# Performance work log

Hardware: AMD Instinct MI355X
Metric: run time of the kernel (lower is better)

## Reference

```python
import jax, jax.numpy as jnp
import numpy as np

B, T, D, P, ALPHA, PR = 4, 4096, 1024, 512, 4, 64


def setup_inputs() -> dict:
    key = jax.random.key(0)
    ks = jax.random.split(key, 9)
    g = lambda k, shape, scale: jax.random.normal(k, shape, jnp.float32) * scale
    return {
        "x": jax.random.normal(ks[0], (B, T, D), jnp.float32),
        "W_toP": g(ks[1], (D, P), D ** -0.5),
        "W_U": g(ks[2], (D, P, ALPHA), D ** -0.5),
        "W_F": g(ks[3], (D, P), D ** -0.5),
        "W_V": g(ks[4], (P, ALPHA), 1.0),
        "W_lam": g(ks[5], (P, PR), P ** -0.5),
        "B_mat": g(ks[6], (P, PR), P ** -0.5),
        "C_mat": g(ks[7], (PR, P), PR ** -0.5),
        "W_fromP": g(ks[8], (P, D), P ** -0.5),
    }


def reference(x, W_toP, W_U, W_F, W_V, W_lam, B_mat, C_mat, W_fromP):
    # dense pre-path: (B,T,D)->(B,T,P)
    pre = jnp.einsum('btd,dp->btp', x, W_toP)
    # CeptaEmbedding dense pathway: multi-factor projection U, gates F, weighted Y
    U = jnp.einsum('btd,dpa->btpa', x, W_U)            # (B,T,P,alpha)
    Fg = jax.nn.sigmoid(jnp.einsum('btd,dp->btp', x, W_F))  # (B,T,P) in (0,1)
    Y = U * W_V                                        # (B,T,P,alpha)
    # CeptaRouting(reduce='sum'): sum over alpha factors, plus residual pre-path
    t = Y.sum(-1) + pre                                # (B,T,P)
    # CeptaSSMLowRank: input-dependent diagonal decay in rank-PR state space
    lam = jax.nn.sigmoid(jnp.einsum('btp,pr->btr', Fg, W_lam))  # (B,T,PR)
    u_in = jnp.einsum('btp,pr->btr', t, B_mat)                  # (B,T,PR)

    def step(s, inp):
        l, u = inp
        s = l * s + u
        return s, s

    s0 = jnp.zeros((x.shape[0], PR), x.dtype)
    _, s_seq = jax.lax.scan(step, s0, (lam.transpose(1, 0, 2), u_in.transpose(1, 0, 2)))
    s_seq = s_seq.transpose(1, 0, 2)                   # (B,T,PR)
    t_tilde = t + jnp.einsum('btr,rp->btp', s_seq, C_mat)
    h = jnp.einsum('btp,pd->btd', t_tilde, W_fromP)    # dropout p=0 -> identity
    return h
```

## Files before the change

kernel.cpp:

```cpp
#include <hip/hip_runtime.h>
#include <hip/hip_bf16.h>

#define Bb 4
#define Tt 4096
#define Dd 1024
#define Pp 512
#define PRr 64
#define Mm (Bb*Tt)
#define NCH 256
#define CL  16

typedef __bf16 bf16;
typedef __bf16 bf16x8 __attribute__((ext_vector_type(8)));
typedef __bf16 bf16x4 __attribute__((ext_vector_type(4)));
typedef float f32x4 __attribute__((ext_vector_type(4)));

#define GPTR(p) (const __attribute__((address_space(1))) void*)(p)
#define LPTR(p) (__attribute__((address_space(3))) void*)(p)

__device__ __forceinline__ float sigmoidf_(float x) {
    return 1.0f / (1.0f + __expf(-x));
}


__global__ void prep_w1(const float* __restrict__ W_toP, const float* __restrict__ W_U,
                        const float* __restrict__ W_V, const float* __restrict__ W_F,
                        bf16* __restrict__ W1t) {
    int idx = blockIdx.x * 256 + threadIdx.x;
    int n = idx >> 10, k = idx & 1023;
    float v;
    if (n < Pp) {
        int p = n;
        float4 u  = *(const float4*)(W_U + ((size_t)k * Pp + p) * 4);
        float4 wv = *(const float4*)(W_V + (size_t)p * 4);
        v = W_toP[(size_t)k * Pp + p] + u.x * wv.x + u.y * wv.y + u.z * wv.z + u.w * wv.w;
    } else {
        v = W_F[(size_t)k * Pp + (n - Pp)];
    }
    W1t[idx] = (bf16)v;
}

__global__ void prep_w3(const float* __restrict__ B_mat, const float* __restrict__ W_lam,
                        bf16* __restrict__ W3t) {
    int idx = blockIdx.x * 256 + threadIdx.x;
    int n = idx >> 10, k = idx & 1023;
    float v = 0.0f;
    if (n < PRr) { if (k < Pp) v = B_mat[(size_t)k * PRr + n]; }
    else         { if (k >= Pp) v = W_lam[(size_t)(k - Pp) * PRr + (n - PRr)]; }
    W3t[idx] = (bf16)v;
}

__global__ void zero_cw(float* __restrict__ CW) {
    int i = blockIdx.x * 256 + threadIdx.x;
    ((f32x4*)CW)[i] = (f32x4){};
}

__global__ void prep_cw(const float* __restrict__ C_mat, const float* __restrict__ W_fromP,
                        float* __restrict__ CW) {
    __shared__ float crow[64];
    int nc = blockIdx.x;
    int r  = blockIdx.y;
    int pc = blockIdx.z;
    int tid = threadIdx.x;
    if (tid < 64) crow[tid] = C_mat[(size_t)r * Pp + pc * 64 + tid];
    __syncthreads();
    int n = nc * 256 + tid;
    float acc = 0.0f;
    #pragma unroll 8
    for (int i = 0; i < 64; ++i)
        acc = fmaf(crow[i], W_fromP[(size_t)(pc * 64 + i) * Dd + n], acc);
    atomicAdd(&CW[(size_t)r * Dd + n], acc);
}

__global__ void prep_w2(const float* __restrict__ W_fromP, const float* __restrict__ CW,
                        bf16* __restrict__ W2t) {
    int n = blockIdx.x;
    int k = threadIdx.x;
    float v = (k < Pp) ? W_fromP[(size_t)k * Dd + n]
                       : CW[(size_t)(k - Pp) * Dd + n];
    W2t[(size_t)n * 576 + k] = (bf16)v;
}

__global__ void cast_x(const float* __restrict__ x, bf16* __restrict__ xb) {
    int i = blockIdx.x * 256 + threadIdx.x;
    float4 v = ((const float4*)x)[i];
    bf16x4 o;
    o[0] = (bf16)v.x; o[1] = (bf16)v.y; o[2] = (bf16)v.z; o[3] = (bf16)v.w;
    ((bf16x4*)xb)[i] = o;
}

__global__ void scan_phase1(const float* __restrict__ UL,
                            float* __restrict__ slocal, float* __restrict__ pprod,
                            float* __restrict__ carryS, float* __restrict__ carryP) {
    int b = blockIdx.y;
    int c = blockIdx.x * 4 + (threadIdx.x >> 6);
    int r = threadIdx.x & 63;
    const float* ulb = UL + ((size_t)b * Tt + (size_t)c * CL) * 128;
    float* sl = slocal + ((size_t)b * Tt + (size_t)c * CL) * PRr;
    float* pp = pprod  + ((size_t)b * Tt + (size_t)c * CL) * PRr;
    float uv[CL], lv[CL];
    #pragma unroll
    for (int i = 0; i < CL; i++) {
        uv[i] = ulb[(size_t)i * 128 + r];
        lv[i] = ulb[(size_t)i * 128 + 64 + r];
    }
    float s = 0.0f, p = 1.0f;
    #pragma unroll
    for (int i = 0; i < CL; i++) {
        s = fmaf(lv[i], s, uv[i]);
        p *= lv[i];
        sl[(size_t)i * PRr + r] = s;
        pp[(size_t)i * PRr + r] = p;
    }
    int ci = b * NCH + c;
    carryS[(size_t)ci * PRr + r] = s;
    carryP[(size_t)ci * PRr + r] = p;
}

__global__ void scan_phase2(const float* __restrict__ carryS, const float* __restrict__ carryP,
                            float* __restrict__ carryIn) {
    int b = blockIdx.x, r = threadIdx.x;
    float carry = 0.0f;
    for (int c0 = 0; c0 < NCH; c0 += 16) {
        float cs[16], cp[16];
        #pragma unroll
        for (int i = 0; i < 16; i++) {
            size_t idx = ((size_t)b * NCH + c0 + i) * PRr + r;
            cs[i] = carryS[idx];
            cp[i] = carryP[idx];
        }
        #pragma unroll
        for (int i = 0; i < 16; i++) {
            carryIn[((size_t)b * NCH + c0 + i) * PRr + r] = carry;
            carry = fmaf(cp[i], carry, cs[i]);
        }
    }
}

__global__ void scan_phase3(const float* __restrict__ slocal, const float* __restrict__ pprod,
                            const float* __restrict__ carryIn, bf16* __restrict__ sb) {
    int i = blockIdx.x * 256 + threadIdx.x;
    int r = i & (PRr - 1);
    int row = i >> 6;
    int b = row >> 12;
    int t = row & (Tt - 1);
    int c = t / CL;
    float carry = carryIn[((size_t)b * NCH + c) * PRr + r];
    sb[i] = (bf16)fmaf(pprod[i], carry, slocal[i]);
}

template <int EPI>
__global__ __launch_bounds__(512, 2) void gemm256(
    const bf16* __restrict__ A0, int lda0,
    const bf16* __restrict__ A1, int lda1, int ksplit,
    const bf16* __restrict__ Bt, int ldb, int K,
    void* __restrict__ Cout, int ldc, int sigcol) {

    __shared__ bf16 As[2][256 * 64];
    __shared__ bf16 Bs[2][256 * 64];

    const int tid  = threadIdx.x;
    const int lane = tid & 63;
    const int wid  = tid >> 6;
    const int wm   = wid >> 2;
    const int wn   = wid & 3;

    const int cpx = gridDim.x >> 3;
    const int bid = blockIdx.x;
    const int swz = (bid & 7) * cpx + (bid >> 3);
    const int mBase = (swz >> 2) * 256;
    const int nBase = (swz & 3) * 256;

    const int lr  = lane & 15;
    const int q16 = (lane >> 4) * 16;

    auto srcA = [&](int kt, const bf16*& src, int& lda, int& kc) {
        if (kt < ksplit) { src = A0; lda = lda0; kc = kt; }
        else             { src = A1; lda = lda1; kc = kt - ksplit; }
    };

    auto stage = [&](const bf16* src, int lda, int kc, int rowBase, bf16* lbuf, int rd) {
        int d = rd * 8192 + tid * 16;
        int L = d ^ (((d >> 7) & 7) << 4);
        int r = L >> 7;
        int c = (L & 127) >> 1;
        const bf16* g = src + (size_t)(rowBase + r) * lda + (kc + c);
        __builtin_amdgcn_global_load_lds(GPTR(g), LPTR((char*)lbuf + d), 16, 0, 0);
    };

    auto frag = [&](const bf16* lbuf, int r, int cb) -> bf16x8 {
        int flat = r * 128 + cb;
        int phys = flat ^ (((flat >> 7) & 7) << 4);
        return *(const bf16x8*)((const char*)lbuf + phys);
    };

    const int NT = K / 64;

    {
        const bf16* sa; int la, kc; srcA(0, sa, la, kc);
        stage(sa, la, kc, mBase, As[0], 0); stage(sa, la, kc, mBase, As[0], 2);
        stage(Bt, ldb, 0, nBase, Bs[0], 0); stage(Bt, ldb, 0, nBase, Bs[0], 1);
        stage(Bt, ldb, 0, nBase, Bs[0], 2); stage(Bt, ldb, 0, nBase, Bs[0], 3);
        stage(sa, la, kc, mBase, As[0], 1); stage(sa, la, kc, mBase, As[0], 3);
    }
    asm volatile("s_waitcnt vmcnt(2)" ::: "memory");
    __builtin_amdgcn_s_barrier();

    f32x4 acc[8][4] = {};
    bf16x8 a[4], b0[4], b1[4];

    for (int t = 0; t < NT; ++t) {
        bf16* Ac = As[t & 1];       bf16* Bc = Bs[t & 1];
        bf16* An = As[(t + 1) & 1]; bf16* Bn = Bs[(t + 1) & 1];
        const bool hn = (t + 1 < NT);
        const bf16* sa = A0; int la = lda0, kc = 0;
        if (hn) srcA((t + 1) * 64, sa, la, kc);
        const int ktn = (t + 1) * 64;

        #pragma unroll
        for (int i = 0; i < 4; ++i) a[i]  = frag(Ac, wm * 128 + i * 16 + lr, q16);
        #pragma unroll
        for (int i = 0; i < 4; ++i) b0[i] = frag(Bc, wn * 64 + i * 16 + lr, q16);
        if (hn) {
            stage(sa, la, kc, mBase, An, 0); stage(sa, la, kc, mBase, An, 2);
            asm volatile("s_waitcnt vmcnt(2)" ::: "memory");
        } else {
            asm volatile("s_waitcnt vmcnt(0)" ::: "memory");
        }
        __builtin_amdgcn_s_barrier();
        __builtin_amdgcn_s_setprio(1);
        #pragma unroll
        for (int m = 0; m < 4; ++m)
            #pragma unroll
            for (int n = 0; n < 4; ++n)
                acc[m][n] = __builtin_amdgcn_mfma_f32_16x16x32_bf16(a[m], b0[n], acc[m][n], 0, 0, 0);
        __builtin_amdgcn_s_setprio(0);
        __builtin_amdgcn_s_barrier();

        #pragma unroll
        for (int i = 0; i < 4; ++i) a[i] = frag(Ac, wm * 128 + (i + 4) * 16 + lr, q16);
        if (hn) { stage(Bt, ldb, ktn, nBase, Bn, 0); stage(Bt, ldb, ktn, nBase, Bn, 1); }
        __builtin_amdgcn_s_barrier();
        __builtin_amdgcn_s_setprio(1);
        #pragma unroll
        for (int m = 0; m < 4; ++m)
            #pragma unroll
            for (int n = 0; n < 4; ++n)
                acc[m + 4][n] = __builtin_amdgcn_mfma_f32_16x16x32_bf16(a[m], b0[n], acc[m + 4][n], 0, 0, 0);
        __builtin_amdgcn_s_setprio(0);
        __builtin_amdgcn_s_barrier();

        #pragma unroll
        for (int i = 0; i < 4; ++i) a[i]  = frag(Ac, wm * 128 + i * 16 + lr, 64 + q16);
        #pragma unroll
        for (int i = 0; i < 4; ++i) b1[i] = frag(Bc, wn * 64 + i * 16 + lr, 64 + q16);
        if (hn) { stage(Bt, ldb, ktn, nBase, Bn, 2); stage(Bt, ldb, ktn, nBase, Bn, 3); }
        __builtin_amdgcn_s_barrier();
        __builtin_amdgcn_s_setprio(1);
        #pragma unroll
        for (int m = 0; m < 4; ++m)
            #pragma unroll
            for (int n = 0; n < 4; ++n)
                acc[m][n] = __builtin_amdgcn_mfma_f32_16x16x32_bf16(a[m], b1[n], acc[m][n], 0, 0, 0);
        __builtin_amdgcn_s_setprio(0);
        __builtin_amdgcn_s_barrier();

        #pragma unroll
        for (int i = 0; i < 4; ++i) a[i] = frag(Ac, wm * 128 + (i + 4) * 16 + lr, 64 + q16);
        if (hn) {
            stage(sa, la, kc, mBase, An, 1); stage(sa, la, kc, mBase, An, 3);
            asm volatile("s_waitcnt vmcnt(2)" ::: "memory");
        }
        __builtin_amdgcn_s_barrier();
        __builtin_amdgcn_s_setprio(1);
        #pragma unroll
        for (int m = 0; m < 4; ++m)
            #pragma unroll
            for (int n = 0; n < 4; ++n)
                acc[m + 4][n] = __builtin_amdgcn_mfma_f32_16x16x32_bf16(a[m], b1[n], acc[m + 4][n], 0, 0, 0);
        __builtin_amdgcn_s_setprio(0);
        __builtin_amdgcn_s_barrier();
    }

    const int lr4 = (lane >> 4) * 4;
    #pragma unroll
    for (int m = 0; m < 8; ++m) {
        #pragma unroll
        for (int n = 0; n < 4; ++n) {
            #pragma unroll
            for (int j = 0; j < 4; ++j) {
                int row = mBase + wm * 128 + m * 16 + lr4 + j;
                int col = nBase + wn * 64 + n * 16 + lr;
                float v = acc[m][n][j];
                if (EPI == 0) {
                    if (col >= sigcol) v = sigmoidf_(v);
                    ((bf16*)Cout)[(size_t)row * ldc + col] = (bf16)v;
                } else {
                    ((float*)Cout)[(size_t)row * ldc + col] = v;
                }
            }
        }
    }
}

template <int EPI>
__global__ __launch_bounds__(256) void gemm_bt(
    const bf16* __restrict__ A0, int lda0,
    const bf16* __restrict__ A1, int lda1, int ksplit,
    const bf16* __restrict__ Bt, int K,
    void* __restrict__ Cout, int ldc, int sigcol) {

    __shared__ bf16 As[128][32];
    __shared__ bf16 Bs[128][32];

    const int tid  = threadIdx.x;
    const int lane = tid & 63;
    const int wid  = tid >> 6;
    const int wr   = (wid >> 1) * 64;
    const int wc   = (wid & 1) * 64;
    const int mBase = blockIdx.x * 128;
    const int nBase = blockIdx.y * 128;

    f32x4 acc[4][4] = {};

    const int lr = lane & 15;
    const int lk = (lane >> 4) * 8;

    for (int kt = 0; kt < K; kt += 32) {
        const bf16* Asrc; int lda_; int kcol;
        if (kt < ksplit) { Asrc = A0; lda_ = lda0; kcol = kt; }
        else             { Asrc = A1; lda_ = lda1; kcol = kt - ksplit; }

        __syncthreads();
        #pragma unroll
        for (int i = 0; i < 2; i++) {
            int c = tid + i * 256;
            int row = c >> 2, k8 = (c & 3) * 8;
            const bf16* g = Asrc + (size_t)(mBase + row) * lda_ + (kcol + k8);
            __builtin_amdgcn_global_load_lds(GPTR(g), LPTR(&As[0][0] + c * 8), 16, 0, 0);
        }
        #pragma unroll
        for (int i = 0; i < 2; i++) {
            int c = tid + i * 256;
            int row = c >> 2, k8 = (c & 3) * 8;
            const bf16* g = Bt + (size_t)(nBase + row) * K + (kt + k8);
            __builtin_amdgcn_global_load_lds(GPTR(g), LPTR(&Bs[0][0] + c * 8), 16, 0, 0);
        }
        __syncthreads();

        bf16x8 af[4], bfr[4];
        #pragma unroll
        for (int m = 0; m < 4; m++) af[m]  = *(const bf16x8*)(&As[wr + m * 16 + lr][lk]);
        #pragma unroll
        for (int n = 0; n < 4; n++) bfr[n] = *(const bf16x8*)(&Bs[wc + n * 16 + lr][lk]);
        #pragma unroll
        for (int m = 0; m < 4; m++)
            #pragma unroll
            for (int n = 0; n < 4; n++)
                acc[m][n] = __builtin_amdgcn_mfma_f32_16x16x32_bf16(af[m], bfr[n], acc[m][n], 0, 0, 0);
    }

    const int lr4 = (lane >> 4) * 4;
    const int lc  = lane & 15;
    #pragma unroll
    for (int m = 0; m < 4; m++) {
        #pragma unroll
        for (int n = 0; n < 4; n++) {
            #pragma unroll
            for (int j = 0; j < 4; j++) {
                int row = mBase + wr + m * 16 + lr4 + j;
                int col = nBase + wc + n * 16 + lc;
                float v = acc[m][n][j];
                if (EPI == 1) {
                    if (col >= sigcol) v = sigmoidf_(v);
                    ((float*)Cout)[(size_t)row * ldc + col] = v;
                } else {
                    ((float*)Cout)[(size_t)row * ldc + col] = v;
                }
            }
        }
    }
}

extern "C" void kernel_launch(void* const* d_in, const int* in_sizes, int n_in,
                              void* d_out, int out_size, void* d_ws, size_t ws_size,
                              hipStream_t stream) {
    const float* x       = (const float*)d_in[0];
    const float* W_toP   = (const float*)d_in[1];
    const float* W_U     = (const float*)d_in[2];
    const float* W_F     = (const float*)d_in[3];
    const float* W_V     = (const float*)d_in[4];
    const float* W_lam   = (const float*)d_in[5];
    const float* B_mat   = (const float*)d_in[6];
    const float* C_mat   = (const float*)d_in[7];
    const float* W_fromP = (const float*)d_in[8];
    float* out = (float*)d_out;

    char* ws = (char*)d_ws;
    size_t off = 0;
    auto alloc = [&](size_t bytes) { void* p = ws + off; off = (off + bytes + 255) & ~255ULL; return p; };
    bf16*  xb  = (bf16*)alloc((size_t)Mm * Dd * 2);
    bf16*  TF  = (bf16*)alloc((size_t)Mm * 1024 * 2);
    float* UL  = (float*)alloc((size_t)Mm * 128 * 4);
    bf16*  sb  = (bf16*)alloc((size_t)Mm * PRr * 2);
    bf16*  W1t = (bf16*)alloc((size_t)1024 * 1024 * 2);
    bf16*  W3t = (bf16*)alloc((size_t)128 * 1024 * 2);
    bf16*  W2t = (bf16*)alloc((size_t)1024 * 576 * 2);
    float* CW  = (float*)alloc((size_t)PRr * Dd * 4);
    float* slocal = (float*)alloc((size_t)Mm * PRr * 4);
    float* pprod  = (float*)alloc((size_t)Mm * PRr * 4);
    float* carryS = (float*)alloc((size_t)Bb * NCH * PRr * 4);
    float* carryP = (float*)alloc((size_t)Bb * NCH * PRr * 4);
    float* carryI = (float*)alloc((size_t)Bb * NCH * PRr * 4);

    prep_w1<<<dim3(4096), dim3(256), 0, stream>>>(W_toP, W_U, W_V, W_F, W1t);
    prep_w3<<<dim3(512),  dim3(256), 0, stream>>>(B_mat, W_lam, W3t);
    zero_cw<<<dim3(64),   dim3(256), 0, stream>>>(CW);
    prep_cw<<<dim3(4, 64, 8), dim3(256), 0, stream>>>(C_mat, W_fromP, CW);
    prep_w2<<<dim3(1024), dim3(576), 0, stream>>>(W_fromP, CW, W2t);
    cast_x <<<dim3(Mm * Dd / 4 / 256), dim3(256), 0, stream>>>(x, xb);

    gemm256<0><<<dim3((Mm / 256) * (1024 / 256)), 512, 0, stream>>>(
        xb, Dd, xb, Dd, 1 << 30, W1t, Dd, Dd, TF, 1024, Pp);

    gemm_bt<1><<<dim3(Mm / 128, 1), 256, 0, stream>>>(
        TF, 1024, TF, 1024, 1 << 30, W3t, 1024, UL, 128, PRr);

    scan_phase1<<<dim3(NCH / 4, Bb), dim3(256), 0, stream>>>(UL, slocal, pprod, carryS, carryP);
    scan_phase2<<<dim3(Bb), dim3(PRr), 0, stream>>>(carryS, carryP, carryI);
    scan_phase3<<<dim3(Mm * PRr / 256), dim3(256), 0, stream>>>(slocal, pprod, carryI, sb);

    gemm256<2><<<dim3((Mm / 256) * (1024 / 256)), 512, 0, stream>>>(
        TF, 1024, sb, PRr, Pp, W2t, 576, 576, out, Dd, 1 << 30);
}
```

Before: 159.1 us.

## Replace 256x256 pipelined GEMM with simpler 128x128 gemm_bt kernel for both big GEMMs

Removes the hand-pipelined 256x256-tile gemm256 kernel and runs the two large GEMMs through the existing 128x128-tile gemm_bt kernel, adding a bf16 sigmoid epilogue variant to it. It also folds the CW zeroing kernel into prep_w3 as extra blocks, saving one launch. The smaller tiles and missing software pipelining likely lower MFMA efficiency and data reuse, in exchange for more blocks and simpler code.

```diff
diff --git a/kernel.cpp b/kernel.cpp
--- a/kernel.cpp
+++ b/kernel.cpp
@@ -41,18 +41,19 @@
 }
 
 __global__ void prep_w3(const float* __restrict__ B_mat, const float* __restrict__ W_lam,
-                        bf16* __restrict__ W3t) {
-    int idx = blockIdx.x * 256 + threadIdx.x;
+                        bf16* __restrict__ W3t, float* __restrict__ CW) {
+    int bid = blockIdx.x;
+    if (bid >= 512) {
+        int i = (bid - 512) * 256 + threadIdx.x;
+        ((f32x4*)CW)[i] = (f32x4){};
+        return;
+    }
+    int idx = bid * 256 + threadIdx.x;
     int n = idx >> 10, k = idx & 1023;
     float v = 0.0f;
     if (n < PRr) { if (k < Pp) v = B_mat[(size_t)k * PRr + n]; }
     else         { if (k >= Pp) v = W_lam[(size_t)(k - Pp) * PRr + (n - PRr)]; }
     W3t[idx] = (bf16)v;
-}
-
-__global__ void zero_cw(float* __restrict__ CW) {
-    int i = blockIdx.x * 256 + threadIdx.x;
-    ((f32x4*)CW)[i] = (f32x4){};
 }
 
 __global__ void prep_cw(const float* __restrict__ C_mat, const float* __restrict__ W_fromP,
@@ -150,160 +151,6 @@
 }
 
 template <int EPI>
-__global__ __launch_bounds__(512, 2) void gemm256(
-    const bf16* __restrict__ A0, int lda0,
-    const bf16* __restrict__ A1, int lda1, int ksplit,
-    const bf16* __restrict__ Bt, int ldb, int K,
-    void* __restrict__ Cout, int ldc, int sigcol) {
-
-    __shared__ bf16 As[2][256 * 64];
-    __shared__ bf16 Bs[2][256 * 64];
-
-    const int tid  = threadIdx.x;
-    const int lane = tid & 63;
-    const int wid  = tid >> 6;
-    const int wm   = wid >> 2;
-    const int wn   = wid & 3;
-
-    const int cpx = gridDim.x >> 3;
-    const int bid = blockIdx.x;
-    const int swz = (bid & 7) * cpx + (bid >> 3);
-    const int mBase = (swz >> 2) * 256;
-    const int nBase = (swz & 3) * 256;
-
-    const int lr  = lane & 15;
-    const int q16 = (lane >> 4) * 16;
-
-    auto srcA = [&](int kt, const bf16*& src, int& lda, int& kc) {
-        if (kt < ksplit) { src = A0; lda = lda0; kc = kt; }
-        else             { src = A1; lda = lda1; kc = kt - ksplit; }
-    };
-
-    auto stage = [&](const bf16* src, int lda, int kc, int rowBase, bf16* lbuf, int rd) {
-        int d = rd * 8192 + tid * 16;
-        int L = d ^ (((d >> 7) & 7) << 4);
-        int r = L >> 7;
-        int c = (L & 127) >> 1;
-        const bf16* g = src + (size_t)(rowBase + r) * lda + (kc + c);
-        __builtin_amdgcn_global_load_lds(GPTR(g), LPTR((char*)lbuf + d), 16, 0, 0);
-    };
-
-    auto frag = [&](const bf16* lbuf, int r, int cb) -> bf16x8 {
-        int flat = r * 128 + cb;
-        int phys = flat ^ (((flat >> 7) & 7) << 4);
-        return *(const bf16x8*)((const char*)lbuf + phys);
-    };
-
-    const int NT = K / 64;
-
-    {
-        const bf16* sa; int la, kc; srcA(0, sa, la, kc);
-        stage(sa, la, kc, mBase, As[0], 0); stage(sa, la, kc, mBase, As[0], 2);
-        stage(Bt, ldb, 0, nBase, Bs[0], 0); stage(Bt, ldb, 0, nBase, Bs[0], 1);
-        stage(Bt, ldb, 0, nBase, Bs[0], 2); stage(Bt, ldb, 0, nBase, Bs[0], 3);
-        stage(sa, la, kc, mBase, As[0], 1); stage(sa, la, kc, mBase, As[0], 3);
-    }
-    asm volatile("s_waitcnt vmcnt(2)" ::: "memory");
-    __builtin_amdgcn_s_barrier();
-
-    f32x4 acc[8][4] = {};
-    bf16x8 a[4], b0[4], b1[4];
-
-    for (int t = 0; t < NT; ++t) {
-        bf16* Ac = As[t & 1];       bf16* Bc = Bs[t & 1];
-        bf16* An = As[(t + 1) & 1]; bf16* Bn = Bs[(t + 1) & 1];
-        const bool hn = (t + 1 < NT);
-        const bf16* sa = A0; int la = lda0, kc = 0;
-        if (hn) srcA((t + 1) * 64, sa, la, kc);
-        const int ktn = (t + 1) * 64;
-
-        #pragma unroll
-        for (int i = 0; i < 4; ++i) a[i]  = frag(Ac, wm * 128 + i * 16 + lr, q16);
-        #pragma unroll
-        for (int i = 0; i < 4; ++i) b0[i] = frag(Bc, wn * 64 + i * 16 + lr, q16);
-        if (hn) {
-            stage(sa, la, kc, mBase, An, 0); stage(sa, la, kc, mBase, An, 2);
-            asm volatile("s_waitcnt vmcnt(2)" ::: "memory");
-        } else {
-            asm volatile("s_waitcnt vmcnt(0)" ::: "memory");
-        }
-        __builtin_amdgcn_s_barrier();
-        __builtin_amdgcn_s_setprio(1);
-        #pragma unroll
-        for (int m = 0; m < 4; ++m)
-            #pragma unroll
-            for (int n = 0; n < 4; ++n)
-                acc[m][n] = __builtin_amdgcn_mfma_f32_16x16x32_bf16(a[m], b0[n], acc[m][n], 0, 0, 0);
-        __builtin_amdgcn_s_setprio(0);
-        __builtin_amdgcn_s_barrier();
-
-        #pragma unroll
-        for (int i = 0; i < 4; ++i) a[i] = frag(Ac, wm * 128 + (i + 4) * 16 + lr, q16);
-        if (hn) { stage(Bt, ldb, ktn, nBase, Bn, 0); stage(Bt, ldb, ktn, nBase, Bn, 1); }
-        __builtin_amdgcn_s_barrier();
-        __builtin_amdgcn_s_setprio(1);
-        #pragma unroll
-        for (int m = 0; m < 4; ++m)
-            #pragma unroll
-            for (int n = 0; n < 4; ++n)
-                acc[m + 4][n] = __builtin_amdgcn_mfma_f32_16x16x32_bf16(a[m], b0[n], acc[m + 4][n], 0, 0, 0);
-        __builtin_amdgcn_s_setprio(0);
-        __builtin_amdgcn_s_barrier();
-
-        #pragma unroll
-        for (int i = 0; i < 4; ++i) a[i]  = frag(Ac, wm * 128 + i * 16 + lr, 64 + q16);
-        #pragma unroll
-        for (int i = 0; i < 4; ++i) b1[i] = frag(Bc, wn * 64 + i * 16 + lr, 64 + q16);
-        if (hn) { stage(Bt, ldb, ktn, nBase, Bn, 2); stage(Bt, ldb, ktn, nBase, Bn, 3); }
-        __builtin_amdgcn_s_barrier();
-        __builtin_amdgcn_s_setprio(1);
-        #pragma unroll
-        for (int m = 0; m < 4; ++m)
-            #pragma unroll
-            for (int n = 0; n < 4; ++n)
-                acc[m][n] = __builtin_amdgcn_mfma_f32_16x16x32_bf16(a[m], b1[n], acc[m][n], 0, 0, 0);
-        __builtin_amdgcn_s_setprio(0);
-        __builtin_amdgcn_s_barrier();
-
-        #pragma unroll
-        for (int i = 0; i < 4; ++i) a[i] = frag(Ac, wm * 128 + (i + 4) * 16 + lr, 64 + q16);
-        if (hn) {
-            stage(sa, la, kc, mBase, An, 1); stage(sa, la, kc, mBase, An, 3);
-            asm volatile("s_waitcnt vmcnt(2)" ::: "memory");
-        }
-        __builtin_amdgcn_s_barrier();
-        __builtin_amdgcn_s_setprio(1);
-        #pragma unroll
-        for (int m = 0; m < 4; ++m)
-            #pragma unroll
-            for (int n = 0; n < 4; ++n)
-                acc[m + 4][n] = __builtin_amdgcn_mfma_f32_16x16x32_bf16(a[m], b1[n], acc[m + 4][n], 0, 0, 0);
-        __builtin_amdgcn_s_setprio(0);
-        __builtin_amdgcn_s_barrier();
-    }
-
-    const int lr4 = (lane >> 4) * 4;
-    #pragma unroll
-    for (int m = 0; m < 8; ++m) {
-        #pragma unroll
-        for (int n = 0; n < 4; ++n) {
-            #pragma unroll
-            for (int j = 0; j < 4; ++j) {
-                int row = mBase + wm * 128 + m * 16 + lr4 + j;
-                int col = nBase + wn * 64 + n * 16 + lr;
-                float v = acc[m][n][j];
-                if (EPI == 0) {
-                    if (col >= sigcol) v = sigmoidf_(v);
-                    ((bf16*)Cout)[(size_t)row * ldc + col] = (bf16)v;
-                } else {
-                    ((float*)Cout)[(size_t)row * ldc + col] = v;
-                }
-            }
-        }
-    }
-}
-
-template <int EPI>
 __global__ __launch_bounds__(256) void gemm_bt(
     const bf16* __restrict__ A0, int lda0,
     const bf16* __restrict__ A1, int lda1, int ksplit,
@@ -371,7 +218,10 @@
                 int row = mBase + wr + m * 16 + lr4 + j;
                 int col = nBase + wc + n * 16 + lc;
                 float v = acc[m][n][j];
-                if (EPI == 1) {
+                if (EPI == 0) {
+                    if (col >= sigcol) v = sigmoidf_(v);
+                    ((bf16*)Cout)[(size_t)row * ldc + col] = (bf16)v;
+                } else if (EPI == 1) {
                     if (col >= sigcol) v = sigmoidf_(v);
                     ((float*)Cout)[(size_t)row * ldc + col] = v;
                 } else {
@@ -414,14 +264,13 @@
     float* carryI = (float*)alloc((size_t)Bb * NCH * PRr * 4);
 
     prep_w1<<<dim3(4096), dim3(256), 0, stream>>>(W_toP, W_U, W_V, W_F, W1t);
-    prep_w3<<<dim3(512),  dim3(256), 0, stream>>>(B_mat, W_lam, W3t);
-    zero_cw<<<dim3(64),   dim3(256), 0, stream>>>(CW);
+    prep_w3<<<dim3(576),  dim3(256), 0, stream>>>(B_mat, W_lam, W3t, CW);
     prep_cw<<<dim3(4, 64, 8), dim3(256), 0, stream>>>(C_mat, W_fromP, CW);
     prep_w2<<<dim3(1024), dim3(576), 0, stream>>>(W_fromP, CW, W2t);
     cast_x <<<dim3(Mm * Dd / 4 / 256), dim3(256), 0, stream>>>(x, xb);
 
-    gemm256<0><<<dim3((Mm / 256) * (1024 / 256)), 512, 0, stream>>>(
-        xb, Dd, xb, Dd, 1 << 30, W1t, Dd, Dd, TF, 1024, Pp);
+    gemm_bt<0><<<dim3(Mm / 128, 1024 / 128), 256, 0, stream>>>(
+        xb, Dd, xb, Dd, 1 << 30, W1t, Dd, TF, 1024, Pp);
 
     gemm_bt<1><<<dim3(Mm / 128, 1), 256, 0, stream>>>(
         TF, 1024, TF, 1024, 1 << 30, W3t, 1024, UL, 128, PRr);
@@ -430,6 +279,6 @@
     scan_phase2<<<dim3(Bb), dim3(PRr), 0, stream>>>(carryS, carryP, carryI);
     scan_phase3<<<dim3(Mm * PRr / 256), dim3(256), 0, stream>>>(slocal, pprod, carryI, sb);
 
-    gemm256<2><<<dim3((Mm / 256) * (1024 / 256)), 512, 0, stream>>>(
-        TF, 1024, sb, PRr, Pp, W2t, 576, 576, out, Dd, 1 << 30);
-}
+    gemm_bt<2><<<dim3(Mm / 128, 1024 / 128), 256, 0, stream>>>(
+        TF, 1024, sb, PRr, Pp, W2t, 576, out, 1024, 1 << 30);
+}
```

Result: slower. 183.3 us (+15.2%).

## Fuse fp32-to-bf16 cast of x into first GEMM's A-operand load path

Applied to the files above, without the earlier changes.

Removes the separate cast_x kernel and the bf16 copy of x. The first GEMM now loads fp32 x into registers, converts it to bf16 and writes it to swizzled LDS, software-pipelined against the MFMA loop. zero_cw is also folded into prep_w3 as extra blocks, saving one launch. The trade-off is that each GEMM block reads twice the A bytes, and each of the 4 N-tile blocks re-reads the same fp32 rows. Register use rises for the staging buffer, and the GEMM gains extra vmcnt(0) waits.

```diff
diff --git a/kernel.cpp b/kernel.cpp
--- a/kernel.cpp
+++ b/kernel.cpp
@@ -41,18 +41,19 @@
 }
 
 __global__ void prep_w3(const float* __restrict__ B_mat, const float* __restrict__ W_lam,
-                        bf16* __restrict__ W3t) {
-    int idx = blockIdx.x * 256 + threadIdx.x;
+                        bf16* __restrict__ W3t, float* __restrict__ CW) {
+    int bid = blockIdx.x;
+    if (bid >= 512) {
+        int i = (bid - 512) * 256 + threadIdx.x;
+        ((f32x4*)CW)[i] = (f32x4){};
+        return;
+    }
+    int idx = bid * 256 + threadIdx.x;
     int n = idx >> 10, k = idx & 1023;
     float v = 0.0f;
     if (n < PRr) { if (k < Pp) v = B_mat[(size_t)k * PRr + n]; }
     else         { if (k >= Pp) v = W_lam[(size_t)(k - Pp) * PRr + (n - PRr)]; }
     W3t[idx] = (bf16)v;
-}
-
-__global__ void zero_cw(float* __restrict__ CW) {
-    int i = blockIdx.x * 256 + threadIdx.x;
-    ((f32x4*)CW)[i] = (f32x4){};
 }
 
 __global__ void prep_cw(const float* __restrict__ C_mat, const float* __restrict__ W_fromP,
@@ -81,14 +82,6 @@
     W2t[(size_t)n * 576 + k] = (bf16)v;
 }
 
-__global__ void cast_x(const float* __restrict__ x, bf16* __restrict__ xb) {
-    int i = blockIdx.x * 256 + threadIdx.x;
-    float4 v = ((const float4*)x)[i];
-    bf16x4 o;
-    o[0] = (bf16)v.x; o[1] = (bf16)v.y; o[2] = (bf16)v.z; o[3] = (bf16)v.w;
-    ((bf16x4*)xb)[i] = o;
-}
-
 __global__ void scan_phase1(const float* __restrict__ UL,
                             float* __restrict__ slocal, float* __restrict__ pprod,
                             float* __restrict__ carryS, float* __restrict__ carryP) {
@@ -149,10 +142,11 @@
     sb[i] = (bf16)fmaf(pprod[i], carry, slocal[i]);
 }
 
-template <int EPI>
+template <int EPI, int AF32>
 __global__ __launch_bounds__(512, 2) void gemm256(
     const bf16* __restrict__ A0, int lda0,
     const bf16* __restrict__ A1, int lda1, int ksplit,
+    const float* __restrict__ Af,
     const bf16* __restrict__ Bt, int ldb, int K,
     void* __restrict__ Cout, int ldc, int sigcol) {
 
@@ -194,16 +188,55 @@
         return *(const bf16x8*)((const char*)lbuf + phys);
     };
 
+    int rrA[4], ccA[4];
+    #pragma unroll
+    for (int rd = 0; rd < 4; ++rd) {
+        int d = rd * 8192 + tid * 16;
+        int L = d ^ (((d >> 7) & 7) << 4);
+        rrA[rd] = L >> 7;
+        ccA[rd] = (L & 127) >> 1;
+    }
+    f32x4 va[8];
+
+    auto issueA = [&](int kc) {
+        #pragma unroll
+        for (int rd = 0; rd < 4; ++rd) {
+            const float* g = Af + (size_t)(mBase + rrA[rd]) * Dd + kc + ccA[rd];
+            va[2 * rd]     = *(const f32x4*)(g);
+            va[2 * rd + 1] = *(const f32x4*)(g + 4);
+        }
+        asm volatile("" ::: "memory");
+    };
+    auto writeA = [&](bf16* lbuf) {
+        #pragma unroll
+        for (int rd = 0; rd < 4; ++rd) {
+            bf16x8 o;
+            #pragma unroll
+            for (int j = 0; j < 4; ++j) {
+                o[j]     = (bf16)va[2 * rd][j];
+                o[j + 4] = (bf16)va[2 * rd + 1][j];
+            }
+            *(bf16x8*)((char*)lbuf + rd * 8192 + tid * 16) = o;
+        }
+    };
+
     const int NT = K / 64;
 
-    {
+    if (AF32) {
+        issueA(0);
+        stage(Bt, ldb, 0, nBase, Bs[0], 0); stage(Bt, ldb, 0, nBase, Bs[0], 1);
+        stage(Bt, ldb, 0, nBase, Bs[0], 2); stage(Bt, ldb, 0, nBase, Bs[0], 3);
+        writeA(As[0]);
+        asm volatile("s_waitcnt lgkmcnt(0)" ::: "memory");
+        asm volatile("s_waitcnt vmcnt(0)" ::: "memory");
+    } else {
         const bf16* sa; int la, kc; srcA(0, sa, la, kc);
         stage(sa, la, kc, mBase, As[0], 0); stage(sa, la, kc, mBase, As[0], 2);
         stage(Bt, ldb, 0, nBase, Bs[0], 0); stage(Bt, ldb, 0, nBase, Bs[0], 1);
         stage(Bt, ldb, 0, nBase, Bs[0], 2); stage(Bt, ldb, 0, nBase, Bs[0], 3);
         stage(sa, la, kc, mBase, As[0], 1); stage(sa, la, kc, mBase, As[0], 3);
-    }
-    asm volatile("s_waitcnt vmcnt(2)" ::: "memory");
+        asm volatile("s_waitcnt vmcnt(2)" ::: "memory");
+    }
     __builtin_amdgcn_s_barrier();
 
     f32x4 acc[8][4] = {};
@@ -214,14 +247,16 @@
         bf16* An = As[(t + 1) & 1]; bf16* Bn = Bs[(t + 1) & 1];
         const bool hn = (t + 1 < NT);
         const bf16* sa = A0; int la = lda0, kc = 0;
-        if (hn) srcA((t + 1) * 64, sa, la, kc);
+        if (!AF32 && hn) srcA((t + 1) * 64, sa, la, kc);
         const int ktn = (t + 1) * 64;
 
         #pragma unroll
         for (int i = 0; i < 4; ++i) a[i]  = frag(Ac, wm * 128 + i * 16 + lr, q16);
         #pragma unroll
         for (int i = 0; i < 4; ++i) b0[i] = frag(Bc, wn * 64 + i * 16 + lr, q16);
-        if (hn) {
+        if (AF32) {
+            if (hn) issueA(ktn);
+        } else if (hn) {
             stage(sa, la, kc, mBase, An, 0); stage(sa, la, kc, mBase, An, 2);
             asm volatile("s_waitcnt vmcnt(2)" ::: "memory");
         } else {
@@ -255,6 +290,10 @@
         #pragma unroll
         for (int i = 0; i < 4; ++i) b1[i] = frag(Bc, wn * 64 + i * 16 + lr, 64 + q16);
         if (hn) { stage(Bt, ldb, ktn, nBase, Bn, 2); stage(Bt, ldb, ktn, nBase, Bn, 3); }
+        if (AF32 && hn) {
+            writeA(An);
+            asm volatile("s_waitcnt lgkmcnt(0)" ::: "memory");
+        }
         __builtin_amdgcn_s_barrier();
         __builtin_amdgcn_s_setprio(1);
         #pragma unroll
@@ -267,7 +306,9 @@
 
         #pragma unroll
         for (int i = 0; i < 4; ++i) a[i] = frag(Ac, wm * 128 + (i + 4) * 16 + lr, 64 + q16);
-        if (hn) {
+        if (AF32) {
+            if (hn) asm volatile("s_waitcnt vmcnt(0)" ::: "memory");
+        } else if (hn) {
             stage(sa, la, kc, mBase, An, 1); stage(sa, la, kc, mBase, An, 3);
             asm volatile("s_waitcnt vmcnt(2)" ::: "memory");
         }
@@ -399,7 +440,6 @@
     char* ws = (char*)d_ws;
     size_t off = 0;
     auto alloc = [&](size_t bytes) { void* p = ws + off; off = (off + bytes + 255) & ~255ULL; return p; };
-    bf16*  xb  = (bf16*)alloc((size_t)Mm * Dd * 2);
     bf16*  TF  = (bf16*)alloc((size_t)Mm * 1024 * 2);
     float* UL  = (float*)alloc((size_t)Mm * 128 * 4);
     bf16*  sb  = (bf16*)alloc((size_t)Mm * PRr * 2);
@@ -414,14 +454,12 @@
     float* carryI = (float*)alloc((size_t)Bb * NCH * PRr * 4);
 
     prep_w1<<<dim3(4096), dim3(256), 0, stream>>>(W_toP, W_U, W_V, W_F, W1t);
-    prep_w3<<<dim3(512),  dim3(256), 0, stream>>>(B_mat, W_lam, W3t);
-    zero_cw<<<dim3(64),   dim3(256), 0, stream>>>(CW);
+    prep_w3<<<dim3(576),  dim3(256), 0, stream>>>(B_mat, W_lam, W3t, CW);
     prep_cw<<<dim3(4, 64, 8), dim3(256), 0, stream>>>(C_mat, W_fromP, CW);
     prep_w2<<<dim3(1024), dim3(576), 0, stream>>>(W_fromP, CW, W2t);
-    cast_x <<<dim3(Mm * Dd / 4 / 256), dim3(256), 0, stream>>>(x, xb);
-
-    gemm256<0><<<dim3((Mm / 256) * (1024 / 256)), 512, 0, stream>>>(
-        xb, Dd, xb, Dd, 1 << 30, W1t, Dd, Dd, TF, 1024, Pp);
+
+    gemm256<0, 1><<<dim3((Mm / 256) * (1024 / 256)), 512, 0, stream>>>(
+        nullptr, 0, nullptr, 0, 1 << 30, x, W1t, Dd, Dd, TF, 1024, Pp);
 
     gemm_bt<1><<<dim3(Mm / 128, 1), 256, 0, stream>>>(
         TF, 1024, TF, 1024, 1 << 30, W3t, 1024, UL, 128, PRr);
@@ -430,6 +468,6 @@
     scan_phase2<<<dim3(Bb), dim3(PRr), 0, stream>>>(carryS, carryP, carryI);
     scan_phase3<<<dim3(Mm * PRr / 256), dim3(256), 0, stream>>>(slocal, pprod, carryI, sb);
 
-    gemm256<2><<<dim3((Mm / 256) * (1024 / 256)), 512, 0, stream>>>(
-        TF, 1024, sb, PRr, Pp, W2t, 576, 576, out, Dd, 1 << 30);
-}
+    gemm256<2, 0><<<dim3((Mm / 256) * (1024 / 256)), 512, 0, stream>>>(
+        TF, 1024, sb, PRr, Pp, nullptr, W2t, 576, 576, out, Dd, 1 << 30);
+}
```

Result: faster. 149.1 us (-6.3%).
